# Performance work log

Measured on AMD Instinct MI355X. Metric: run time of the kernel, lower is better.

## Reference

```python
import jax, jax.numpy as jnp
import numpy as np

B, Q, WAY, SHOT, H, W, C = 2, 75, 5, 5, 10, 10, 640
NEIGHBOR_K = 5


def setup_inputs() -> dict:
    key = jax.random.key(0)
    k1, k2 = jax.random.split(key)
    input1 = jax.random.normal(k1, (B, Q, H, W, C), dtype=jnp.float32)
    # per the original unpacking: dim1=shot, dim2=way
    input2 = jax.random.normal(k2, (B, SHOT, WAY, H, W, C), dtype=jnp.float32)
    return {"input1": input1, "input2": input2, "neighbor_k": NEIGHBOR_K}


def reference(input1, input2, neighbor_k):
    # input1: [b, q_num, h, w, c] query local descriptors
    # input2: [b, shot, way, h, w, c] support local descriptors
    b, q_num, h, w, c = input1.shape
    _, shot, way, _, _, _ = input2.shape
    hw = h * w

    q = input1.reshape(b, q_num, hw, c)
    s = input2.reshape(b, way * shot, hw, c)

    # L2-normalize each local descriptor over channel dim
    q = q / jnp.linalg.norm(q, axis=-1, keepdims=True)
    s = s / jnp.linalg.norm(s, axis=-1, keepdims=True)

    # group support descriptors per class: [b, way, shot*hw, c]
    # (matches torch .view semantics on the contiguous flattened buffer)
    support = s.reshape(b, way, shot * hw, c)

    # cosine similarity between every query patch and every support patch
    # scores: [b, q_num, way, hw, shot*hw]
    scores = jnp.einsum('bqpc,bwsc->bqwps', q, support)

    # top-k nearest support descriptors per query patch, mean over k
    topv, _ = jax.lax.top_k(scores, neighbor_k)          # [b,q,way,hw,k]
    sim_local = jnp.sum(topv, axis=-1) / neighbor_k      # [b,q,way,hw]
    sim_way = jnp.sum(sim_local, axis=-1)                # [b,q,way]
    return sim_way
```

## Files before the change

### kernel.cpp

```cpp
#include <hip/hip_runtime.h>

#define QN    75
#define HWN   100
#define CN    640
#define NSUP  500
#define MROWS 7500
#define NQD   (2 * MROWS)
#define NSD   5000
#define NDESC (NQD + NSD)
#define MT    128
#define NT    256
#define BK    64
#define CST   272

typedef __attribute__((ext_vector_type(8))) __bf16 bf16x8;
typedef __attribute__((ext_vector_type(4))) float  f32x4;

#define GLDS(gp, lp) __builtin_amdgcn_global_load_lds(                        \
    (const __attribute__((address_space(1))) void*)(gp),                      \
    (__attribute__((address_space(3))) void*)(lp), 16, 0, 0)

static __device__ inline unsigned short f2bf(float f) {
    unsigned int u = __float_as_uint(f);
    u += 0x7fffu + ((u >> 16) & 1u);
    return (unsigned short)(u >> 16);
}

__global__ __launch_bounds__(256) void prep_kernel(const float* __restrict__ q,
                                                   const float* __restrict__ s,
                                                   unsigned short* __restrict__ qbf,
                                                   unsigned short* __restrict__ sbf) {
    int wave = (blockIdx.x * 256 + threadIdx.x) >> 6;
    int lane = threadIdx.x & 63;
    if (wave >= NDESC) return;
    const float* src = (wave < NQD) ? (q + (size_t)wave * CN)
                                    : (s + (size_t)(wave - NQD) * CN);
    unsigned short* dst = (wave < NQD) ? (qbf + (size_t)wave * CN)
                                       : (sbf + (size_t)(wave - NQD) * CN);
    float4 v[3];
    float ss = 0.f;
#pragma unroll
    for (int j = 0; j < 3; ++j) {
        int idx4 = lane + 64 * j;
        if (idx4 < CN / 4) {
            v[j] = *(const float4*)(src + idx4 * 4);
            ss = fmaf(v[j].x, v[j].x, ss);
            ss = fmaf(v[j].y, v[j].y, ss);
            ss = fmaf(v[j].z, v[j].z, ss);
            ss = fmaf(v[j].w, v[j].w, ss);
        }
    }
#pragma unroll
    for (int off = 32; off > 0; off >>= 1)
        ss += __shfl_xor(ss, off, 64);
    float inv = rsqrtf(ss);
#pragma unroll
    for (int j = 0; j < 3; ++j) {
        int idx4 = lane + 64 * j;
        if (idx4 < CN / 4) {
            ushort4 o;
            o.x = f2bf(v[j].x * inv);
            o.y = f2bf(v[j].y * inv);
            o.z = f2bf(v[j].z * inv);
            o.w = f2bf(v[j].w * inv);
            *(ushort4*)(dst + idx4 * 4) = o;
        }
    }
}

__global__ __launch_bounds__(512, 4) void mfma_kernel(const unsigned short* __restrict__ qbf,
                                                      const unsigned short* __restrict__ sbf,
                                                      float* __restrict__ part) {
    const int xcd = blockIdx.x & 7;
    const int idx = blockIdx.x >> 3;
    const int b   = xcd >> 2;
    const int mbq = xcd & 3;
    const int mbsz = (mbq < 3) ? 15 : 14;
    if (idx >= 10 * mbsz) return;
    const int g  = idx / (2 * mbsz);
    const int r_ = idx % (2 * mbsz);
    const int nc = r_ / mbsz;
    const int mb = mbq * 15 + (r_ % mbsz);
    const int bg = b * 5 + g;
    const int r0 = mb * MT;
    const int c0 = nc * NT;

    __shared__ __align__(16) char smem[49152];
    unsigned short* Alds = (unsigned short*)smem;
    unsigned short* Blds = (unsigned short*)(smem + 16384);
    float*          Cst  = (float*)smem;

    const int t    = threadIdx.x;
    const int lane = t & 63;
    const int wid  = t >> 6;
    const int h    = wid >> 2;
    const int colq = wid & 3;

    const unsigned short* qptr = qbf + (size_t)b * MROWS * CN;
    const unsigned short* sptr = sbf + (size_t)(b * 25 + g * 5) * HWN * CN;

    f32x4 acc[4][4];
#pragma unroll
    for (int mt = 0; mt < 4; ++mt)
#pragma unroll
        for (int nt = 0; nt < 4; ++nt)
            acc[mt][nt] = (f32x4)0.f;

    const int lx   = lane >> 3;
    const int ls   = lane & 7;
    const int gsrc = ls ^ lx;

    int ar0 = r0 + wid * 16 + lx;       if (ar0 > MROWS - 1) ar0 = MROWS - 1;
    int ar1 = r0 + wid * 16 + 8 + lx;   if (ar1 > MROWS - 1) ar1 = MROWS - 1;
    const int aoff0 = ar0 * CN + gsrc * 8;
    const int aoff1 = ar1 * CN + gsrc * 8;
    char* aldst = smem + wid * 2048;

    int boff[4];
#pragma unroll
    for (int c = 0; c < 4; ++c) {
        int col = c0 + wid * 32 + c * 8 + lx;
        if (col > NSUP - 1) col = NSUP - 1;
        boff[c] = col * CN + gsrc * 8;
    }
    char* bldst = smem + 16384 + wid * 4096;

    const int q_ = lane >> 4;
    const int lr = lane & 15;
    const int sw = lr & 7;

    for (int k0 = 0; k0 < CN; k0 += BK) {
        __syncthreads();
        GLDS(qptr + aoff0 + k0, aldst);
        GLDS(qptr + aoff1 + k0, aldst + 1024);
#pragma unroll
        for (int c = 0; c < 4; ++c)
            GLDS(sptr + boff[c] + k0, bldst + c * 1024);
        __syncthreads();

#pragma unroll
        for (int ks = 0; ks < 2; ++ks) {
            const int sl = ((ks * 4 + q_) ^ sw) * 8;
            bf16x8 af[4];
#pragma unroll
            for (int mt = 0; mt < 4; ++mt)
                af[mt] = *(const bf16x8*)(Alds + (h * 64 + mt * 16 + lr) * 64 + sl);
#pragma unroll
            for (int nt = 0; nt < 4; ++nt) {
                bf16x8 bfr = *(const bf16x8*)(Blds + (colq * 64 + nt * 16 + lr) * 64 + sl);
#pragma unroll
                for (int mt = 0; mt < 4; ++mt)
                    acc[mt][nt] = __builtin_amdgcn_mfma_f32_16x16x32_bf16(af[mt], bfr, acc[mt][nt], 0, 0, 0);
            }
        }
    }

    const int erow = t >> 4;
    const int es   = t & 15;
#define CE(a, b) { float hi_ = fmaxf(a, b), lo_ = fminf(a, b); a = hi_; b = lo_; }
#pragma unroll
    for (int mt = 0; mt < 4; ++mt) {
        __syncthreads();
#pragma unroll
        for (int nt = 0; nt < 4; ++nt)
#pragma unroll
            for (int e = 0; e < 4; ++e)
                Cst[(h * 16 + q_ * 4 + e) * CST + colq * 64 + nt * 16 + lr] = acc[mt][nt][e];
        __syncthreads();

        float t0 = -3.4e38f, t1 = -3.4e38f, t2 = -3.4e38f, t3 = -3.4e38f, t4 = -3.4e38f;
#pragma unroll
        for (int i = 0; i < 16; ++i) {
            int col = es + 16 * i;
            float v = (c0 + col < NSUP) ? Cst[erow * CST + col] : -3.4e38f;
            float hi;
            hi = fmaxf(t0, v); v = fminf(t0, v); t0 = hi;
            hi = fmaxf(t1, v); v = fminf(t1, v); t1 = hi;
            hi = fmaxf(t2, v); v = fminf(t2, v); t2 = hi;
            hi = fmaxf(t3, v); v = fminf(t3, v); t3 = hi;
            hi = fmaxf(t4, v); v = fminf(t4, v); t4 = hi;
        }
#pragma unroll
        for (int d = 1; d < 16; d <<= 1) {
            float b0 = __shfl_xor(t0, d, 64);
            float b1 = __shfl_xor(t1, d, 64);
            float b2 = __shfl_xor(t2, d, 64);
            float b3 = __shfl_xor(t3, d, 64);
            float b4 = __shfl_xor(t4, d, 64);
            t0 = fmaxf(t0, b4); t1 = fmaxf(t1, b3); t2 = fmaxf(t2, b2);
            t3 = fmaxf(t3, b1); t4 = fmaxf(t4, b0);
            CE(t0, t1); CE(t2, t3);
            CE(t1, t2); CE(t3, t4);
            CE(t0, t1); CE(t2, t3);
            CE(t1, t2); CE(t3, t4);
            CE(t0, t1); CE(t2, t3);
        }
        if (es == 0) {
            int patch = r0 + (erow >> 4) * 64 + mt * 16 + (erow & 15);
            if (patch < MROWS) {
                float* pp = part + ((size_t)(bg * MROWS + patch) * 2 + nc) * 5;
                pp[0] = t0; pp[1] = t1; pp[2] = t2; pp[3] = t3; pp[4] = t4;
            }
        }
    }
#undef CE
}

__global__ __launch_bounds__(256) void merge_kernel(const float* __restrict__ part,
                                                    float* __restrict__ out) {
    int w    = (blockIdx.x * 256 + threadIdx.x) >> 6;
    int lane = threadIdx.x & 63;
    if (w >= 750) return;
    int b  = w / 375, r = w % 375;
    int qi = r / 5,   g = r % 5;
    int bg = b * 5 + g;

    float sum = 0.f;
    for (int p = lane; p < HWN; p += 64) {
        int row = qi * HWN + p;
        const float* pp = part + (size_t)(bg * MROWS + row) * 10;
        float t0 = -3.4e38f, t1 = -3.4e38f, t2 = -3.4e38f, t3 = -3.4e38f, t4 = -3.4e38f;
#pragma unroll
        for (int j = 0; j < 10; ++j) {
            float v = pp[j], hi;
            hi = fmaxf(t0, v); v = fminf(t0, v); t0 = hi;
            hi = fmaxf(t1, v); v = fminf(t1, v); t1 = hi;
            hi = fmaxf(t2, v); v = fminf(t2, v); t2 = hi;
            hi = fmaxf(t3, v); v = fminf(t3, v); t3 = hi;
            hi = fmaxf(t4, v); v = fminf(t4, v); t4 = hi;
        }
        sum += (t0 + t1 + t2 + t3 + t4) * 0.2f;
    }
#pragma unroll
    for (int off = 32; off > 0; off >>= 1)
        sum += __shfl_xor(sum, off, 64);
    if (lane == 0) out[w] = sum;
}

extern "C" void kernel_launch(void* const* d_in, const int* in_sizes, int n_in,
                              void* d_out, int out_size, void* d_ws, size_t ws_size,
                              hipStream_t stream) {
    const float* in1 = (const float*)d_in[0];
    const float* in2 = (const float*)d_in[1];
    float* out = (float*)d_out;

    unsigned short* qbf  = (unsigned short*)d_ws;
    unsigned short* sbf  = qbf + (size_t)NQD * CN;
    float*          part = (float*)(sbf + (size_t)NSD * CN);

    prep_kernel<<<dim3(NDESC / 4), 256, 0, stream>>>(in1, in2, qbf, sbf);
    mfma_kernel<<<dim3(1200), 512, 0, stream>>>(qbf, sbf, part);
    merge_kernel<<<dim3(188), 256, 0, stream>>>(part, out);
}
```

Before: 159.6 us.

## Double-buffer LDS tiles to overlap global loads with MFMA compute

The K loop now uses two LDS buffers: the next K tile is issued via global_load_lds into one buffer while MFMAs consume the other, leaving one barrier per iteration instead of two. The aim is to hide global load latency that the old single-buffered loop exposed between barriers. In exchange, LDS use doubles to 96KB per block and launch bounds drop from 4 to 2 blocks per CU, which lowers occupancy. The loop is restructured with a prologue stage and an epilogue compute.

```diff
diff --git a/kernel.cpp b/kernel.cpp
--- a/kernel.cpp
+++ b/kernel.cpp
@@ -12,6 +12,7 @@
 #define NT    256
 #define BK    64
 #define CST   272
+#define BUFSZ 49152
 
 typedef __attribute__((ext_vector_type(8))) __bf16 bf16x8;
 typedef __attribute__((ext_vector_type(4))) float  f32x4;
@@ -68,7 +69,7 @@
     }
 }
 
-__global__ __launch_bounds__(512, 4) void mfma_kernel(const unsigned short* __restrict__ qbf,
+__global__ __launch_bounds__(512, 2) void mfma_kernel(const unsigned short* __restrict__ qbf,
                                                       const unsigned short* __restrict__ sbf,
                                                       float* __restrict__ part) {
     const int xcd = blockIdx.x & 7;
@@ -85,10 +86,8 @@
     const int r0 = mb * MT;
     const int c0 = nc * NT;
 
-    __shared__ __align__(16) char smem[49152];
-    unsigned short* Alds = (unsigned short*)smem;
-    unsigned short* Blds = (unsigned short*)(smem + 16384);
-    float*          Cst  = (float*)smem;
+    __shared__ __align__(16) char smem[2 * BUFSZ];
+    float* Cst = (float*)smem;
 
     const int t    = threadIdx.x;
     const int lane = t & 63;
@@ -114,7 +113,6 @@
     int ar1 = r0 + wid * 16 + 8 + lx;   if (ar1 > MROWS - 1) ar1 = MROWS - 1;
     const int aoff0 = ar0 * CN + gsrc * 8;
     const int aoff1 = ar1 * CN + gsrc * 8;
-    char* aldst = smem + wid * 2048;
 
     int boff[4];
 #pragma unroll
@@ -123,37 +121,56 @@
         if (col > NSUP - 1) col = NSUP - 1;
         boff[c] = col * CN + gsrc * 8;
     }
-    char* bldst = smem + 16384 + wid * 4096;
 
     const int q_ = lane >> 4;
     const int lr = lane & 15;
     const int sw = lr & 7;
 
-    for (int k0 = 0; k0 < CN; k0 += BK) {
+#define STAGE(base, kk)                                                        \
+    {                                                                          \
+        char* ad = smem + (base) + wid * 2048;                                 \
+        char* bd = smem + (base) + 16384 + wid * 4096;                         \
+        GLDS(qptr + aoff0 + (kk), ad);                                         \
+        GLDS(qptr + aoff1 + (kk), ad + 1024);                                  \
+        GLDS(sptr + boff[0] + (kk), bd);                                       \
+        GLDS(sptr + boff[1] + (kk), bd + 1024);                                \
+        GLDS(sptr + boff[2] + (kk), bd + 2048);                                \
+        GLDS(sptr + boff[3] + (kk), bd + 3072);                                \
+    }
+
+#define COMPUTE(base)                                                          \
+    {                                                                          \
+        const unsigned short* Al = (const unsigned short*)(smem + (base));     \
+        const unsigned short* Bl = (const unsigned short*)(smem + (base) + 16384); \
+        _Pragma("unroll")                                                      \
+        for (int ks = 0; ks < 2; ++ks) {                                       \
+            const int sl = ((ks * 4 + q_) ^ sw) * 8;                           \
+            bf16x8 af[4];                                                      \
+            _Pragma("unroll")                                                  \
+            for (int mt = 0; mt < 4; ++mt)                                     \
+                af[mt] = *(const bf16x8*)(Al + (h * 64 + mt * 16 + lr) * 64 + sl); \
+            _Pragma("unroll")                                                  \
+            for (int nt = 0; nt < 4; ++nt) {                                   \
+                bf16x8 bfr = *(const bf16x8*)(Bl + (colq * 64 + nt * 16 + lr) * 64 + sl); \
+                _Pragma("unroll")                                              \
+                for (int mt = 0; mt < 4; ++mt)                                 \
+                    acc[mt][nt] = __builtin_amdgcn_mfma_f32_16x16x32_bf16(af[mt], bfr, acc[mt][nt], 0, 0, 0); \
+            }                                                                  \
+        }                                                                      \
+    }
+
+    STAGE(0, 0);
+    __syncthreads();
+#pragma unroll 2
+    for (int kt = 0; kt < 9; ++kt) {
+        const int cb = (kt & 1) * BUFSZ;
+        STAGE(BUFSZ - cb, (kt + 1) * BK);
+        COMPUTE(cb);
         __syncthreads();
-        GLDS(qptr + aoff0 + k0, aldst);
-        GLDS(qptr + aoff1 + k0, aldst + 1024);
-#pragma unroll
-        for (int c = 0; c < 4; ++c)
-            GLDS(sptr + boff[c] + k0, bldst + c * 1024);
-        __syncthreads();
-
-#pragma unroll
-        for (int ks = 0; ks < 2; ++ks) {
-            const int sl = ((ks * 4 + q_) ^ sw) * 8;
-            bf16x8 af[4];
-#pragma unroll
-            for (int mt = 0; mt < 4; ++mt)
-                af[mt] = *(const bf16x8*)(Alds + (h * 64 + mt * 16 + lr) * 64 + sl);
-#pragma unroll
-            for (int nt = 0; nt < 4; ++nt) {
-                bf16x8 bfr = *(const bf16x8*)(Blds + (colq * 64 + nt * 16 + lr) * 64 + sl);
-#pragma unroll
-                for (int mt = 0; mt < 4; ++mt)
-                    acc[mt][nt] = __builtin_amdgcn_mfma_f32_16x16x32_bf16(af[mt], bfr, acc[mt][nt], 0, 0, 0);
-            }
-        }
-    }
+    }
+    COMPUTE(BUFSZ);
+#undef STAGE
+#undef COMPUTE
 
     const int erow = t >> 4;
     const int es   = t & 15;
```

Result: slower. 169.1 us (+6.0%).
